# Performance work log

Hardware: AMD Instinct MI355X
Metric: run time of the kernel (lower is better)

## Reference

```python
import jax, jax.numpy as jnp
import numpy as np

NUM_CLASSES = 19
VIEWS = 50          # views_per_class: min(min_views, max_views_per_class)=50, no max_features_total cap (38*50<=10000)
TEMP = 0.1
CM_TEMP = 0.1
EPS = 1e-12


def setup_inputs() -> dict:
    key = jax.random.key(0)
    k1, k2, k3 = jax.random.split(key, 3)
    label = jax.random.randint(k1, (2, 512, 1024), 0, NUM_CLASSES)
    color_fea = jax.random.normal(k2, (2, 256, 128, 256), dtype=jnp.float32)
    other_fea = jax.random.normal(k3, (2, 256, 128, 256), dtype=jnp.float32)
    return {"label": label, "color_fea": color_fea, "other_fea": other_fea}


def _sample(compare, feature):
    # compare: [N, Cc, HW] bool (pixel belongs to class), feature: [N, C, HW]
    # random per-class sampling of VIEWS pixels: argsort random keys restricted to class pixels
    n, cc, hw = compare.shape
    rand = jax.random.uniform(jax.random.key(42), (n, hw))
    keys = jnp.where(compare, rand[:, None, :], 2.0)          # non-class pixels pushed to the end
    idx = jnp.argsort(keys, axis=-1)[:, :, :VIEWS]            # [N, Cc, V]
    samp = jnp.take_along_axis(feature[:, None, :, :], idx[:, :, None, :], axis=-1)  # [N, Cc, C, V]
    c = feature.shape[1]
    return samp.reshape(n * cc, c, VIEWS)                     # [T, C, V]


def _norm_flat(feats):
    # feats: [T, C, V] -> l2-normalize over C, transpose, flatten to [T*V, C]
    f = feats / jnp.maximum(jnp.linalg.norm(feats, axis=1, keepdims=True), EPS)
    t, c, v = f.shape
    return jnp.transpose(f, (0, 2, 1)).reshape(t * v, c)


def _masks(labels_flat):
    m = (labels_flat[:, None] == labels_flat[None, :]).astype(jnp.float32)
    neg = 1.0 - m
    pos = m * (1.0 - jnp.eye(m.shape[0], dtype=m.dtype))      # exclude self from positives
    return pos, neg


def _infonce(dot, pos, neg):
    exp = jnp.exp(dot)
    neg_logits = (exp * neg).sum(1, keepdims=True)
    log_prob = dot - jnp.log(exp + neg_logits)
    pos_sums = pos.sum(1)
    norm = jnp.where(pos_sums > 0, pos_sums, 1.0)
    return -(((pos * log_prob).sum(1)) / norm).mean()


def reference(label, color_fea, other_fea):
    n, h, w = label.shape
    scale = w // color_fea.shape[-1]
    # nearest-neighbour downsample of label to feature resolution (torch interpolate 'nearest' with integer factor)
    ld = label[:, ::scale, ::scale].reshape(n, -1)                       # [N, HW]
    compare = ld[:, None, :] == jnp.arange(NUM_CLASSES)[None, :, None]   # [N, Cc, HW]
    cf = color_fea.reshape(n, color_fea.shape[1], -1)
    of = other_fea.reshape(n, other_fea.shape[1], -1)
    fc = _sample(compare, cf)                                            # [T, C, V]
    fo = _sample(compare, of)
    labels = jnp.tile(jnp.arange(NUM_CLASSES), n).astype(jnp.float32)    # [T]
    labels_flat = jnp.repeat(labels, VIEWS)                              # [T*V]
    pos, neg = _masks(labels_flat)
    fcf = _norm_flat(fc)
    fof = _norm_flat(fo)
    loss_cm = _infonce(fcf @ fof.T / CM_TEMP, pos, neg)
    loss_vis = _infonce(fcf @ fcf.T / TEMP, pos, neg)
    loss_aux = _infonce(fof @ fof.T / TEMP, pos, neg)
    return (loss_cm, loss_vis, loss_aux)
```

## Files before the change

### kernel.cpp

```cpp
#include <hip/hip_runtime.h>
#include <hip/hip_bf16.h>
#include <cstdint>
#include <cstddef>

#define HW    32768
#define NCLS  19
#define VIEWS 50
#define NT    38
#define NR    1900
#define NRP   1920
#define CH    256
#define CAP   3072

#define OFF_RAND 0u
#define OFF_LD   65536u
#define OFF_SEL  131072u
#define OFF_CNT  133120u
#define OFF_KEYS 133184u
#define OFF_FCF  366656u
#define OFF_FOF  612416u
#define OFF_NEG  858176u
#define OFF_POS  863936u

typedef __attribute__((ext_vector_type(8))) short short8;
typedef __attribute__((ext_vector_type(4))) float f32x4;

__device__ __forceinline__ unsigned rotl32(unsigned x, int d) {
    return (x << d) | (x >> (32 - d));
}

__device__ __forceinline__ void async_copy16(const void* g, void* l) {
    __builtin_amdgcn_global_load_lds(
        (const __attribute__((address_space(1))) unsigned int*)g,
        (__attribute__((address_space(3))) unsigned int*)l, 16, 0, 0);
}

__global__ __launch_bounds__(256) void prep_kernel(const int* __restrict__ label,
                                                   float* __restrict__ rnd,
                                                   int* __restrict__ ld,
                                                   int* __restrict__ counts,
                                                   unsigned long long* __restrict__ keys,
                                                   float* __restrict__ negsum) {
    int tid = threadIdx.x;
    int j = blockIdx.x * 256 + tid;
    unsigned x0 = (unsigned)j, x1 = (unsigned)(j + HW);
    const unsigned ks0 = 0u, ks1 = 42u, ks2 = 0x1BD11BDAu ^ 0u ^ 42u;
    x0 += ks0; x1 += ks1;
#define TF_RND(r) { x0 += x1; x1 = rotl32(x1, r); x1 ^= x0; }
    TF_RND(13) TF_RND(15) TF_RND(26) TF_RND(6)   x0 += ks1; x1 += ks2 + 1u;
    TF_RND(17) TF_RND(29) TF_RND(16) TF_RND(24)  x0 += ks2; x1 += ks0 + 2u;
    TF_RND(13) TF_RND(15) TF_RND(26) TF_RND(6)   x0 += ks0; x1 += ks1 + 3u;
    TF_RND(17) TF_RND(29) TF_RND(16) TF_RND(24)  x0 += ks1; x1 += ks2 + 4u;
    TF_RND(13) TF_RND(15) TF_RND(26) TF_RND(6)   x0 += ks2; x1 += ks0 + 5u;
#undef TF_RND
    float r0 = __uint_as_float((x0 >> 9) | 0x3f800000u) - 1.0f;
    float r1 = __uint_as_float((x1 >> 9) | 0x3f800000u) - 1.0f;
    rnd[j]      = r0;
    rnd[HW + j] = r1;
    int y = j >> 8, x = j & 255;
    int off = (y << 2) * 1024 + (x << 2);
    int c0 = label[off];
    int c1 = label[512 * 1024 + off];
    ld[j]      = c0;
    ld[HW + j] = c1;
    if (j < 3 * NR) negsum[j] = 0.0f;

    __shared__ int lcnt[NT], lbase[NT];
    if (tid < NT) lcnt[tid] = 0;
    __syncthreads();
    int t0 = c0, t1 = NCLS + c1;
    int p0 = atomicAdd(&lcnt[t0], 1);
    int p1 = atomicAdd(&lcnt[t1], 1);
    __syncthreads();
    if (tid < NT) {
        int c = lcnt[tid];
        lbase[tid] = (c > 0) ? atomicAdd(&counts[tid], c) : 0;
    }
    __syncthreads();
    int s0 = lbase[t0] + p0;
    int s1 = lbase[t1] + p1;
    if (s0 < CAP)
        keys[(size_t)t0 * CAP + s0] = (((unsigned long long)__float_as_uint(r0)) << 32) | (unsigned)j;
    if (s1 < CAP)
        keys[(size_t)t1 * CAP + s1] = (((unsigned long long)__float_as_uint(r1)) << 32) | (unsigned)j;
}

__global__ __launch_bounds__(256) void select_kernel(const int* __restrict__ counts,
                                                     const unsigned long long* __restrict__ keys,
                                                     const int* __restrict__ ld,
                                                     int* __restrict__ sel) {
    int t = blockIdx.x;
    int tid = threadIdx.x;
    int cnt = min(counts[t], CAP);
    const unsigned long long* g = keys + (size_t)t * CAP;
    __shared__ unsigned hist[256];
    __shared__ unsigned long long cand[256];
    __shared__ int s_B, s_nbelow, s_ncand;
    hist[tid] = 0;
    if (tid == 0) { s_B = 256; s_nbelow = 0; s_ncand = 0; }
    __syncthreads();

    unsigned long long kreg[12];
    int binreg[12];
    int nk = 0;
    for (int p = tid; p < cnt; p += 256) {
        unsigned long long k = g[p];
        unsigned v = (unsigned)(__uint_as_float((unsigned)(k >> 32)) * 8388608.0f);
        int b = (int)(v >> 15);
        kreg[nk] = k; binreg[nk] = b; nk++;
        atomicAdd(&hist[b], 1u);
    }
    __syncthreads();

    if (cnt >= VIEWS) {
        for (int s = 1; s < 256; s <<= 1) {
            unsigned add = (tid >= s) ? hist[tid - s] : 0u;
            unsigned cur = hist[tid];
            __syncthreads();
            hist[tid] = cur + add;
            __syncthreads();
        }
        unsigned cum  = hist[tid];
        unsigned prev = (tid > 0) ? hist[tid - 1] : 0u;
        if (cum >= VIEWS && prev < VIEWS) s_B = tid;
        __syncthreads();
        int B = s_B;
        for (int q = 0; q < nk; ++q) {
            if (binreg[q] < B) {
                int pos = atomicAdd(&s_nbelow, 1);
                if (pos < VIEWS) sel[t * VIEWS + pos] = (int)(kreg[q] & 0xffffffffu);
            } else if (binreg[q] == B) {
                int pos = atomicAdd(&s_ncand, 1);
                if (pos < 256) cand[pos] = kreg[q];
            }
        }
        __syncthreads();
        int nbelow = s_nbelow;
        int need   = VIEWS - nbelow;
        int ncand  = min(s_ncand, 256);
        if (tid < 64) {
            unsigned long long r0 = (tid       < ncand) ? cand[tid]       : ~0ull;
            unsigned long long r1 = (tid + 64  < ncand) ? cand[tid + 64]  : ~0ull;
            unsigned long long r2 = (tid + 128 < ncand) ? cand[tid + 128] : ~0ull;
            unsigned long long r3 = (tid + 192 < ncand) ? cand[tid + 192] : ~0ull;
            for (int v = 0; v < need; ++v) {
                unsigned long long a = (r0 < r1) ? r0 : r1;
                unsigned long long b = (r2 < r3) ? r2 : r3;
                unsigned long long best = (a < b) ? a : b;
                for (int m = 32; m >= 1; m >>= 1) {
                    unsigned long long o = __shfl_xor(best, m);
                    if (o < best) best = o;
                }
                if (tid == 0) sel[t * VIEWS + nbelow + v] = (int)(best & 0xffffffffu);
                if (r0 == best) r0 = ~0ull;
                if (r1 == best) r1 = ~0ull;
                if (r2 == best) r2 = ~0ull;
                if (r3 == best) r3 = ~0ull;
            }
        }
    } else {
        for (int q = 0; q < nk; ++q) {
            int pos = atomicAdd(&s_nbelow, 1);
            if (pos < VIEWS) sel[t * VIEWS + pos] = (int)(kreg[q] & 0xffffffffu);
        }
        __syncthreads();
        if (tid == 0) {
            int fill = s_nbelow;
            int n = t / NCLS, c = t % NCLS;
            const int* ldn = ld + n * HW;
            for (int j = 0; j < HW && fill < VIEWS; ++j)
                if (ldn[j] != c) sel[t * VIEWS + fill++] = j;
        }
    }
}

__global__ __launch_bounds__(256) void gather_kernel(const float* __restrict__ cf,
                                                     const float* __restrict__ of,
                                                     const int* __restrict__ sel,
                                                     unsigned short* __restrict__ fcf,
                                                     unsigned short* __restrict__ fof) {
    int r = blockIdx.x;
    int ch = threadIdx.x;
    if (r >= NR) {
        fcf[r * CH + ch] = 0;
        fof[r * CH + ch] = 0;
        return;
    }
    int t = r / VIEWS;
    int n = t / NCLS;
    int idx = sel[r];
    float vc = cf[(size_t)(n * CH + ch) * HW + idx];
    float vo = of[(size_t)(n * CH + ch) * HW + idx];
    __shared__ float partc[4], parto[4];
    float sc = vc * vc, so = vo * vo;
    for (int m = 32; m >= 1; m >>= 1) {
        sc += __shfl_xor(sc, m);
        so += __shfl_xor(so, m);
    }
    int wave = ch >> 6, lane = ch & 63;
    if (lane == 0) { partc[wave] = sc; parto[wave] = so; }
    __syncthreads();
    float nc = fmaxf(sqrtf(partc[0] + partc[1] + partc[2] + partc[3]), 1e-12f);
    float no = fmaxf(sqrtf(parto[0] + parto[1] + parto[2] + parto[3]), 1e-12f);
    __hip_bfloat16 hc = __float2bfloat16(vc / nc);
    __hip_bfloat16 ho = __float2bfloat16(vo / no);
    fcf[r * CH + ch] = *(unsigned short*)&hc;
    fof[r * CH + ch] = *(unsigned short*)&ho;
}

__global__ __launch_bounds__(256) void gram_kernel(const unsigned short* __restrict__ fcf,
                                                   const unsigned short* __restrict__ fof,
                                                   float* __restrict__ negsum,
                                                   float* __restrict__ posdot) {
    int z = blockIdx.z;
    const unsigned short* A = (z == 2) ? fof : fcf;
    const unsigned short* B = (z == 1) ? fcf : fof;
    int i0 = blockIdx.y * 64, j0 = blockIdx.x * 64;
    int tid = threadIdx.x;
    int wave = tid >> 6, lane = tid & 63;
    __shared__ unsigned short As[64][32], Bs[64][32];
    __shared__ float negs[64];
    if (tid < 64) negs[tid] = 0.0f;
    f32x4 acc[4] = {{0,0,0,0},{0,0,0,0},{0,0,0,0},{0,0,0,0}};
    int srow = wave * 16 + (lane >> 2);
    int scol = (lane & 3) * 8;
    const unsigned short* ga = A + (size_t)(i0 + srow) * CH + scol;
    const unsigned short* gb = B + (size_t)(j0 + srow) * CH + scol;
    unsigned short* la = &As[wave * 16][0];
    unsigned short* lb = &Bs[wave * 16][0];
    int arow = wave * 16 + (lane & 15);
    int koff = (lane >> 4) * 8;
    for (int kc = 0; kc < CH; kc += 32) {
        async_copy16(ga + kc, la);
        async_copy16(gb + kc, lb);
        __syncthreads();
        short8 af = *(const short8*)&As[arow][koff];
        for (int b = 0; b < 4; ++b) {
            short8 bf = *(const short8*)&Bs[b * 16 + (lane & 15)][koff];
            acc[b] = __builtin_amdgcn_mfma_f32_16x16x32_bf16(af, bf, acc[b], 0, 0, 0);
        }
        __syncthreads();
    }
    float* pd = posdot + (size_t)z * NR * 100;
    int col = lane & 15, quad = lane >> 4;
    for (int r = 0; r < 4; ++r) {
        int irow = wave * 16 + quad * 4 + r;
        int i = i0 + irow;
        bool iok = (i < NR);
        int ci = (i / VIEWS) % NCLS;
        float negacc = 0.0f;
        for (int b = 0; b < 4; ++b) {
            int j = j0 + b * 16 + col;
            if (!iok || j >= NR) continue;
            int cj = (j / VIEWS) % NCLS;
            float d = acc[b][r] * 10.0f;
            if (ci == cj) {
                int p = (j / (NCLS * VIEWS)) * VIEWS + (j % VIEWS);
                pd[(size_t)i * 100 + p] = d;
            } else {
                negacc += __expf(d);
            }
        }
        for (int m = 8; m >= 1; m >>= 1) negacc += __shfl_xor(negacc, m);
        if (col == 0 && iok) negs[irow] = negacc;
    }
    __syncthreads();
    if (tid < 64) {
        int i = i0 + tid;
        if (i < NR) atomicAdd(&negsum[z * NR + i], negs[tid]);
    }
}

__global__ void finalize_kernel(const float* __restrict__ negsum,
                                const float* __restrict__ posdot,
                                float* __restrict__ out) {
    int g = blockIdx.x * 256 + threadIdx.x;
    __shared__ float part[3];
    if (threadIdx.x < 3) part[threadIdx.x] = 0.0f;
    __syncthreads();
    if (g < 3 * NR) {
        int l = g / NR, i = g % NR;
        float NL = negsum[l * NR + i];
        int pself = (i / (NCLS * VIEWS)) * VIEWS + (i % VIEWS);
        const float* pd = posdot + ((size_t)l * NR + i) * 100;
        float s = 0.0f;
        for (int p = 0; p < 100; ++p) {
            if (p == pself) continue;
            float d = pd[p];
            s += d - logf(__expf(d) + NL);
        }
        atomicAdd(&part[l], s);
    }
    __syncthreads();
    if (threadIdx.x < 3)
        atomicAdd(&out[threadIdx.x], -part[threadIdx.x] * (1.0f / (99.0f * 1900.0f)));
}

extern "C" void kernel_launch(void* const* d_in, const int* in_sizes, int n_in,
                              void* d_out, int out_size, void* d_ws, size_t ws_size,
                              hipStream_t stream) {
    (void)in_sizes; (void)n_in; (void)out_size; (void)ws_size;
    const int*   label = (const int*)d_in[0];
    const float* cf    = (const float*)d_in[1];
    const float* of    = (const float*)d_in[2];
    float* ws = (float*)d_ws;
    float*              rnd    = ws + OFF_RAND;
    int*                ld     = (int*)(ws + OFF_LD);
    int*                sel    = (int*)(ws + OFF_SEL);
    int*                counts = (int*)(ws + OFF_CNT);
    unsigned long long* keys   = (unsigned long long*)(ws + OFF_KEYS);
    unsigned short*     fcf    = (unsigned short*)(ws + OFF_FCF);
    unsigned short*     fof    = (unsigned short*)(ws + OFF_FOF);
    float*              negsum = ws + OFF_NEG;
    float*              posdot = ws + OFF_POS;
    float*              out    = (float*)d_out;

    hipMemsetAsync(counts, 0, NT * sizeof(int), stream);
    hipMemsetAsync(out, 0, 3 * sizeof(float), stream);

    prep_kernel<<<HW / 256, 256, 0, stream>>>(label, rnd, ld, counts, keys, negsum);
    select_kernel<<<NT, 256, 0, stream>>>(counts, keys, ld, sel);
    gather_kernel<<<NRP, 256, 0, stream>>>(cf, of, sel, fcf, fof);
    dim3 g4(NRP / 64, NRP / 64, 3);
    gram_kernel<<<g4, 256, 0, stream>>>(fcf, fof, negsum, posdot);
    finalize_kernel<<<(3 * NR + 255) / 256, 256, 0, stream>>>(negsum, posdot, out);
}
```

Before: 208.5 us.

## Exploit Gram symmetry for self-similarity losses and drop unused random buffer

For the two self-similarity Gram matrices (fcf·fcfᵀ and fof·fofᵀ), blocks below the diagonal now return early. Upper off-diagonal blocks also write the mirrored positive dot products and add the mirrored negative exp-sums for the column rows. This roughly halves the MFMA work for two of the three Gram slices, at the cost of extra scattered writes and atomics. It also removes the unused random-number stores and folds the output memset into the prep kernel, saving one memset launch.

Measured after the change: 205.0 us. Within noise of the previous version (-1.7%).

```diff
diff --git a/kernel.cpp b/kernel.cpp
--- a/kernel.cpp
+++ b/kernel.cpp
@@ -12,7 +12,6 @@
 #define CH    256
 #define CAP   3072
 
-#define OFF_RAND 0u
 #define OFF_LD   65536u
 #define OFF_SEL  131072u
 #define OFF_CNT  133120u
@@ -36,11 +35,11 @@
 }
 
 __global__ __launch_bounds__(256) void prep_kernel(const int* __restrict__ label,
-                                                   float* __restrict__ rnd,
                                                    int* __restrict__ ld,
                                                    int* __restrict__ counts,
                                                    unsigned long long* __restrict__ keys,
-                                                   float* __restrict__ negsum) {
+                                                   float* __restrict__ negsum,
+                                                   float* __restrict__ out) {
     int tid = threadIdx.x;
     int j = blockIdx.x * 256 + tid;
     unsigned x0 = (unsigned)j, x1 = (unsigned)(j + HW);
@@ -55,8 +54,6 @@
 #undef TF_RND
     float r0 = __uint_as_float((x0 >> 9) | 0x3f800000u) - 1.0f;
     float r1 = __uint_as_float((x1 >> 9) | 0x3f800000u) - 1.0f;
-    rnd[j]      = r0;
-    rnd[HW + j] = r1;
     int y = j >> 8, x = j & 255;
     int off = (y << 2) * 1024 + (x << 2);
     int c0 = label[off];
@@ -64,6 +61,7 @@
     ld[j]      = c0;
     ld[HW + j] = c1;
     if (j < 3 * NR) negsum[j] = 0.0f;
+    if (j < 3) out[j] = 0.0f;
 
     __shared__ int lcnt[NT], lbase[NT];
     if (tid < NT) lcnt[tid] = 0;
@@ -213,14 +211,17 @@
                                                    float* __restrict__ negsum,
                                                    float* __restrict__ posdot) {
     int z = blockIdx.z;
+    bool sym = (z >= 1);
+    if (sym && blockIdx.y > blockIdx.x) return;
+    bool mirror = sym && (blockIdx.y < blockIdx.x);
     const unsigned short* A = (z == 2) ? fof : fcf;
     const unsigned short* B = (z == 1) ? fcf : fof;
     int i0 = blockIdx.y * 64, j0 = blockIdx.x * 64;
     int tid = threadIdx.x;
     int wave = tid >> 6, lane = tid & 63;
     __shared__ unsigned short As[64][32], Bs[64][32];
-    __shared__ float negs[64];
-    if (tid < 64) negs[tid] = 0.0f;
+    __shared__ float negs[64], negsB[64];
+    if (tid < 64) { negs[tid] = 0.0f; negsB[tid] = 0.0f; }
     f32x4 acc[4] = {{0,0,0,0},{0,0,0,0},{0,0,0,0},{0,0,0,0}};
     int srow = wave * 16 + (lane >> 2);
     int scol = (lane & 3) * 8;
@@ -243,6 +244,7 @@
     }
     float* pd = posdot + (size_t)z * NR * 100;
     int col = lane & 15, quad = lane >> 4;
+    float negB[4] = {0.0f, 0.0f, 0.0f, 0.0f};
     for (int r = 0; r < 4; ++r) {
         int irow = wave * 16 + quad * 4 + r;
         int i = i0 + irow;
@@ -257,17 +259,35 @@
             if (ci == cj) {
                 int p = (j / (NCLS * VIEWS)) * VIEWS + (j % VIEWS);
                 pd[(size_t)i * 100 + p] = d;
+                if (mirror) {
+                    int q = (i / (NCLS * VIEWS)) * VIEWS + (i % VIEWS);
+                    pd[(size_t)j * 100 + q] = d;
+                }
             } else {
-                negacc += __expf(d);
+                float e = __expf(d);
+                negacc += e;
+                if (mirror) negB[b] += e;
             }
         }
         for (int m = 8; m >= 1; m >>= 1) negacc += __shfl_xor(negacc, m);
         if (col == 0 && iok) negs[irow] = negacc;
+    }
+    if (mirror) {
+        for (int b = 0; b < 4; ++b) {
+            float v = negB[b];
+            v += __shfl_xor(v, 16);
+            v += __shfl_xor(v, 32);
+            if (quad == 0) atomicAdd(&negsB[b * 16 + col], v);
+        }
     }
     __syncthreads();
     if (tid < 64) {
         int i = i0 + tid;
         if (i < NR) atomicAdd(&negsum[z * NR + i], negs[tid]);
+        if (mirror) {
+            int j = j0 + tid;
+            if (j < NR) atomicAdd(&negsum[z * NR + j], negsB[tid]);
+        }
     }
 }
 
@@ -304,7 +324,6 @@
     const float* cf    = (const float*)d_in[1];
     const float* of    = (const float*)d_in[2];
     float* ws = (float*)d_ws;
-    float*              rnd    = ws + OFF_RAND;
     int*                ld     = (int*)(ws + OFF_LD);
     int*                sel    = (int*)(ws + OFF_SEL);
     int*                counts = (int*)(ws + OFF_CNT);
@@ -316,9 +335,8 @@
     float*              out    = (float*)d_out;
 
     hipMemsetAsync(counts, 0, NT * sizeof(int), stream);
-    hipMemsetAsync(out, 0, 3 * sizeof(float), stream);
-
-    prep_kernel<<<HW / 256, 256, 0, stream>>>(label, rnd, ld, counts, keys, negsum);
+
+    prep_kernel<<<HW / 256, 256, 0, stream>>>(label, ld, counts, keys, negsum, out);
     select_kernel<<<NT, 256, 0, stream>>>(counts, keys, ld, sel);
     gather_kernel<<<NRP, 256, 0, stream>>>(cf, of, sel, fcf, fof);
     dim3 g4(NRP / 64, NRP / 64, 3);
```
